# Performance work log

Measured on AMD Instinct MI355X. Metric: run time of the kernel, lower is better.

Reference implementation:

```python
import jax, jax.numpy as jnp
import numpy as np

# cfg.SIAMESE constants (typical FastVOD values)
ROIS_PER_IMAGE = 128
FG_PER_IMAGE = 32          # round(0.25 * 128)
FG_THRESH = 0.7
BG_THRESH_HI = 0.3
BG_THRESH_LO = 0.0

B, N, G = 16, 65536, 64


def _make_boxes(key, shape, img=1000.0):
    k1, k2, k3, k4 = jax.random.split(key, 4)
    x1 = jax.random.uniform(k1, shape) * (img - 64.0)
    y1 = jax.random.uniform(k2, shape) * (img - 64.0)
    w = jax.random.uniform(k3, shape) * 200.0 + 8.0
    h = jax.random.uniform(k4, shape) * 200.0 + 8.0
    return jnp.stack([x1, y1, jnp.minimum(x1 + w, img), jnp.minimum(y1 + h, img)], axis=-1)


def setup_inputs() -> dict:
    key = jax.random.key(0)
    kr, kg, kl, kt, kp, kf, kb, km = jax.random.split(key, 8)
    roi_boxes = _make_boxes(kr, (B, N))                      # [B,N,4]
    all_rois = jnp.concatenate([jnp.zeros((B, N, 1)), roi_boxes], axis=-1)  # [B,N,5]
    gtb = _make_boxes(kg, (B, G))                            # [B,G,4]
    labels = jax.random.randint(kl, (B, G), 1, 31).astype(jnp.float32)
    tids = jax.random.randint(kt, (B, G), 0, 1000).astype(jnp.float32)
    # pad last 8 gt per image with zero boxes (common padding pattern)
    pad = jnp.arange(G) >= G - 8
    gtb = jnp.where(pad[None, :, None], 0.0, gtb)
    labels = jnp.where(pad[None, :], 0.0, labels)
    gt_boxes = jnp.concatenate([gtb, labels[..., None], tids[..., None]], axis=-1)  # [B,G,6]
    u_perm = jax.random.uniform(kp, (B, N + G))
    u_fg = jax.random.uniform(kf, (B, ROIS_PER_IMAGE))
    u_bg = jax.random.uniform(kb, (B, ROIS_PER_IMAGE))
    return {"all_rois": all_rois, "gt_boxes": gt_boxes, "u_perm": u_perm,
            "u_fg": u_fg, "u_bg": u_bg}


def _bbox_overlaps_batch(rois, gt):
    # rois: [B,Nt,5] (idx,x1,y1,x2,y2), gt: [B,G,4]
    a = rois[:, :, 1:5]
    aw = a[:, :, 2] - a[:, :, 0] + 1.0
    ah = a[:, :, 3] - a[:, :, 1] + 1.0
    gw = gt[:, :, 2] - gt[:, :, 0] + 1.0
    gh = gt[:, :, 3] - gt[:, :, 1] + 1.0
    area_a = aw * ah                                  # [B,Nt]
    area_g = gw * gh                                  # [B,G]
    iw = jnp.clip(jnp.minimum(a[:, :, None, 2], gt[:, None, :, 2])
                  - jnp.maximum(a[:, :, None, 0], gt[:, None, :, 0]) + 1.0, 0.0)
    ih = jnp.clip(jnp.minimum(a[:, :, None, 3], gt[:, None, :, 3])
                  - jnp.maximum(a[:, :, None, 1], gt[:, None, :, 1]) + 1.0, 0.0)
    inter = iw * ih                                   # [B,Nt,G]
    ov = inter / (area_a[:, :, None] + area_g[:, None, :] - inter)
    gt_zero = (gw == 1.0) & (gh == 1.0)
    a_zero = (aw == 1.0) & (ah == 1.0)
    ov = jnp.where(gt_zero[:, None, :], 0.0, ov)
    ov = jnp.where(a_zero[:, :, None], -1.0, ov)
    return ov


def _sample_one(max_ov, up, uf, ub):
    # max_ov: [Nt]; replicates the per-image fg/bg sampling loop, vectorized.
    R = ROIS_PER_IMAGE
    fg_mask = max_ov >= FG_THRESH
    bg_mask = ((max_ov < BG_THRESH_HI) & (max_ov >= BG_THRESH_LO)) | (max_ov < 0)
    fg_num = fg_mask.sum()
    bg_num = bg_mask.sum()
    # randomly-ordered fg (resp. bg) indices come first after the argsort
    fg_order = jnp.argsort(jnp.where(fg_mask, up, 2.0))
    bg_order = jnp.argsort(jnp.where(bg_mask, up, 2.0))
    both = (fg_num > 0) & (bg_num > 0)
    only_fg = (fg_num > 0) & (bg_num == 0)
    fg_this = jnp.where(both, jnp.minimum(FG_PER_IMAGE, fg_num),
                        jnp.where(only_fg, R, 0))
    pos = jnp.arange(R)
    # fg: permutation (no replacement) when both present, else uniform w/ replacement
    fg_repl = jnp.clip((uf * fg_num).astype(jnp.int32), 0, jnp.maximum(fg_num - 1, 0))
    fg_pick = jnp.where(only_fg, fg_order[fg_repl], fg_order[pos])
    # bg: always uniform with replacement
    bg_repl = jnp.clip((ub * bg_num).astype(jnp.int32), 0, jnp.maximum(bg_num - 1, 0))
    bg_pick = bg_order[bg_repl]
    is_fg = pos < fg_this
    keep = jnp.where(is_fg, fg_pick, bg_pick)
    return keep, is_fg


def reference(all_rois, gt_boxes, u_perm, u_fg, u_bg):
    # append gt boxes as proposals: [B, N+G, 5]
    gt_append = jnp.concatenate(
        [jnp.zeros_like(gt_boxes[:, :, :1]), gt_boxes[:, :, :4]], axis=-1)
    rois_all = jnp.concatenate([all_rois, gt_append], axis=1)
    ov = _bbox_overlaps_batch(rois_all, gt_boxes[:, :, :4])      # [B,Nt,G]
    max_ov = jnp.max(ov, axis=2)
    gt_assign = jnp.argmax(ov, axis=2)                            # [B,Nt]
    labels = jnp.take_along_axis(gt_boxes[:, :, 4], gt_assign, axis=1)   # [B,Nt]
    tids = jnp.take_along_axis(gt_boxes[:, :, 5], gt_assign, axis=1)
    keep, is_fg = jax.vmap(_sample_one)(max_ov, u_perm, u_fg, u_bg)      # [B,R]
    lab_b = jnp.where(is_fg, jnp.take_along_axis(labels, keep, axis=1), 0.0)
    tid_b = jnp.where(is_fg, jnp.take_along_axis(tids, keep, axis=1), -1.0)
    rois_b = jnp.take_along_axis(rois_all, keep[:, :, None], axis=1)     # [B,R,5]
    batch_idx = jnp.arange(rois_b.shape[0], dtype=rois_b.dtype)[:, None]
    rois_b = rois_b.at[:, :, 0].set(jnp.broadcast_to(batch_idx, rois_b.shape[:2]))
    return rois_b, lab_b, tid_b
```

## Files before the change

### kernel.cpp

```cpp
#include <hip/hip_runtime.h>

#define B_   16
#define N_   65536
#define G_   64
#define M_   (N_ + G_)
#define R_   128
#define FGP  32
#define NB_  16384
#define NCH_ 32
#define CHUNK_ (NB_ / NCH_)
#define NROW_ (B_ * 2)
#define FW_  (NB_ / 32)

__global__ void prep_kernel(const float* __restrict__ gt_boxes,
                            float* __restrict__ gtp)
{
    int t = blockIdx.x * blockDim.x + threadIdx.x;
    if (t >= B_ * G_) return;
    int b = t / G_, j = t % G_;
    const float* g = gt_boxes + t * 6;
    float x1 = g[0], y1 = g[1], x2 = g[2], y2 = g[3];
    float gw = x2 - x1 + 1.0f, gh = y2 - y1 + 1.0f;
    float area = gw * gh;
    bool gz = (gw == 1.0f) && (gh == 1.0f);
    float* o = gtp + b * 5 * G_;
    o[0 * G_ + j] = gz ?  3.0e8f : x1;
    o[1 * G_ + j] = gz ?  3.0e8f : y1;
    o[2 * G_ + j] = gz ? -3.0e8f : x2;
    o[3 * G_ + j] = gz ? -3.0e8f : y2;
    o[4 * G_ + j] = area;
}

__global__ void iou_kernel(const float* __restrict__ all_rois,
                           const float* __restrict__ gt_boxes,
                           const float* __restrict__ gtp,
                           const float* __restrict__ u_perm,
                           unsigned*    __restrict__ packed,
                           int*         __restrict__ hist)
{
    const int b = blockIdx.y;
    const int i = blockIdx.x * blockDim.x + threadIdx.x;
    if (i >= M_) return;

    float x1, y1, x2, y2;
    if (i < N_) {
        const float* p = all_rois + ((size_t)b * N_ + i) * 5;
        x1 = p[1]; y1 = p[2]; x2 = p[3]; y2 = p[4];
    } else {
        const float* p = gt_boxes + (b * G_ + (i - N_)) * 6;
        x1 = p[0]; y1 = p[1]; x2 = p[2]; y2 = p[3];
    }
    float aw = x2 - x1 + 1.0f, ah = y2 - y1 + 1.0f;
    float area_a = aw * ah;
    bool  a_zero = (aw == 1.0f) && (ah == 1.0f);

    const float* gp = gtp + b * 5 * G_;
    float ib = 0.0f, ub = 1.0f;
    #pragma unroll 16
    for (int j = 0; j < G_; ++j) {
        float iw = fminf(x2, gp[2 * G_ + j]) - fmaxf(x1, gp[0 * G_ + j]) + 1.0f;
        float ih = fminf(y2, gp[3 * G_ + j]) - fmaxf(y1, gp[1 * G_ + j]) + 1.0f;
        iw = fmaxf(iw, 0.0f);
        ih = fmaxf(ih, 0.0f);
        float inter = iw * ih;
        float uni   = area_a + gp[4 * G_ + j] - inter;
        float hi1 = inter * ub;
        float lo1 = fmaf(inter, ub, -hi1);
        float hi2 = ib * uni;
        float lo2 = fmaf(ib, uni, -hi2);
        bool gt = (hi1 > hi2) || ((hi1 == hi2) && (lo1 > lo2));
        if (gt) { ib = inter; ub = uni; }
    }
    float best = ib / ub;
    if (a_zero) best = -1.0f;

    bool fg = best >= 0.7f;
    bool bg = best < 0.3f;
    unsigned pk = 0xFFFFFFFFu;
    if (fg || bg) {
        int cls = fg ? 0 : 1;
        float u = u_perm[(size_t)b * M_ + i];
        int bucket = min(max((int)(u * (float)NB_), 0), NB_ - 1);
        pk = ((unsigned)cls << 16) | (unsigned)bucket;
        atomicAdd(&hist[(size_t)(b * 2 + cls) * NB_ + bucket], 1);
    }
    packed[(size_t)b * M_ + i] = pk;
}

__global__ void scan_row(int* __restrict__ hist,
                         int* __restrict__ coarse,
                         int* __restrict__ cnt)
{
    __shared__ int bs[512];
    const int row = blockIdx.x, t = threadIdx.x;
    int4* h4 = (int4*)(hist + (size_t)row * NB_ + t * 32);
    int v[32];
    #pragma unroll
    for (int k = 0; k < 8; ++k) {
        int4 x = h4[k];
        v[k * 4 + 0] = x.x; v[k * 4 + 1] = x.y;
        v[k * 4 + 2] = x.z; v[k * 4 + 3] = x.w;
    }
    int run = 0;
    #pragma unroll
    for (int k = 0; k < 32; ++k) { int x = v[k]; v[k] = run; run += x; }
    bs[t] = run;
    __syncthreads();
    for (int d = 1; d < 512; d <<= 1) {
        int add = (t >= d) ? bs[t - d] : 0;
        __syncthreads();
        bs[t] += add;
        __syncthreads();
    }
    const int texcl = bs[t] - run;
    if ((t & 15) == 15) coarse[row * NCH_ + (t >> 4)] = bs[t];
    if (t == 511) cnt[row] = bs[511];
    #pragma unroll
    for (int k = 0; k < 8; ++k) {
        int4 x;
        x.x = v[k * 4 + 0] + texcl; x.y = v[k * 4 + 1] + texcl;
        x.z = v[k * 4 + 2] + texcl; x.w = v[k * 4 + 3] + texcl;
        h4[k] = x;
    }
}

__global__ void flag_kernel(const float* __restrict__ u_fg,
                            const float* __restrict__ u_bg,
                            const int*  __restrict__ cnt,
                            const int*  __restrict__ coarse,
                            const int*  __restrict__ E,
                            unsigned*   __restrict__ flags,
                            int4*       __restrict__ pick)
{
    __shared__ int sc[2 * NCH_];
    const int b = blockIdx.x;
    const int pos = threadIdx.x;
    if (pos < 2 * NCH_) sc[pos] = coarse[(b * 2) * NCH_ + pos];
    __syncthreads();

    const int fgn = cnt[b * 2 + 0];
    const int bgn = cnt[b * 2 + 1];
    const bool both    = (fgn > 0) && (bgn > 0);
    const bool only_fg = (fgn > 0) && (bgn == 0);
    const int fg_this  = both ? min(FGP, fgn) : (only_fg ? R_ : 0);
    const bool is_fg   = pos < fg_this;

    int cls, rank, cnum;
    if (is_fg) {
        cls = 0; cnum = fgn;
        if (only_fg) {
            float uf = u_fg[b * R_ + pos];
            int kk = (int)(uf * (float)fgn);
            rank = min(max(kk, 0), max(fgn - 1, 0));
        } else {
            rank = pos;
        }
    } else {
        cls = 1; cnum = bgn;
        float ubv = u_bg[b * R_ + pos];
        int kk = (int)(ubv * (float)bgn);
        rank = min(max(kk, 0), max(bgn - 1, 0));
    }

    int4 pk4 = make_int4(0, 0, 0, 0);
    if (cnum > 0) {
        const int row = b * 2 + cls;
        const int* sce = sc + cls * NCH_;
        int c = 0;
        while (c < NCH_ - 1 && sce[c] <= rank) ++c;
        const int* Er = E + (size_t)row * NB_;
        int lo = c * CHUNK_, hi = c * CHUNK_ + CHUNK_ - 1;
        while (lo < hi) {
            int mid = (lo + hi + 1) >> 1;
            if (Er[mid] <= rank) lo = mid; else hi = mid - 1;
        }
        const int start = Er[lo];
        const int next  = (lo < NB_ - 1) ? Er[lo + 1] : cnum;
        atomicOr(&flags[row * FW_ + (lo >> 5)], 1u << (lo & 31));
        pk4 = make_int4(start, next - start, rank - start, lo);
    }
    pick[b * R_ + pos] = pk4;
}

__global__ void scatter_kernel(const unsigned* __restrict__ packed,
                               const unsigned* __restrict__ flags,
                               int*            __restrict__ E,
                               int*            __restrict__ buckets)
{
    const int b = blockIdx.y;
    const int i = blockIdx.x * blockDim.x + threadIdx.x;
    if (i >= M_) return;
    unsigned pk = packed[(size_t)b * M_ + i];
    if (pk == 0xFFFFFFFFu) return;
    const int cls = (int)(pk >> 16);
    const int bucket = (int)(pk & 0xFFFFu);
    const int row = b * 2 + cls;
    unsigned w = flags[row * FW_ + (bucket >> 5)];
    if (!(w & (1u << (bucket & 31)))) return;
    int p = atomicAdd(&E[(size_t)row * NB_ + bucket], 1);
    buckets[(size_t)row * M_ + p] = i;
}

__global__ void sample_kernel(const float* __restrict__ all_rois,
                              const float* __restrict__ gt_boxes,
                              const float* __restrict__ gtp,
                              const float* __restrict__ u_perm,
                              const int*  __restrict__ cnt,
                              const int4* __restrict__ pick,
                              const int*  __restrict__ buckets,
                              float*      __restrict__ out)
{
    const int b   = blockIdx.x;
    const int pos = threadIdx.x;
    const int fgn = cnt[b * 2 + 0];
    const int bgn = cnt[b * 2 + 1];
    const bool both    = (fgn > 0) && (bgn > 0);
    const bool only_fg = (fgn > 0) && (bgn == 0);
    const int fg_this  = both ? min(FGP, fgn) : (only_fg ? R_ : 0);
    const bool is_fg   = pos < fg_this;
    const int cls  = is_fg ? 0 : 1;

    const int4 pk = pick[b * R_ + pos];
    int keep = 0;
    if (pk.y > 0) {
        const int row = b * 2 + cls;
        const int*   be = buckets + (size_t)row * M_ + pk.x;
        const float* up = u_perm + (size_t)b * M_;
        const int cnt2 = pk.y, r = pk.z;
        for (int t2 = 0; t2 < cnt2; ++t2) {
            int it = be[t2]; float ut = up[it];
            int rk = 0;
            for (int s2 = 0; s2 < cnt2; ++s2) {
                if (s2 == t2) continue;
                int is2 = be[s2]; float us = up[is2];
                if (us < ut || (us == ut && is2 < it)) rk++;
            }
            if (rk == r) { keep = it; break; }
        }
    }

    float ox1, oy1, ox2, oy2;
    if (keep < N_) {
        const float* p = all_rois + ((size_t)b * N_ + keep) * 5;
        ox1 = p[1]; oy1 = p[2]; ox2 = p[3]; oy2 = p[4];
    } else {
        const float* p = gt_boxes + (b * G_ + (keep - N_)) * 6;
        ox1 = p[0]; oy1 = p[1]; ox2 = p[2]; oy2 = p[3];
    }
    float* ro = out + ((size_t)b * R_ + pos) * 5;
    ro[0] = (float)b; ro[1] = ox1; ro[2] = oy1; ro[3] = ox2; ro[4] = oy2;

    float lab = 0.0f, tidv = -1.0f;
    if (is_fg) {
        float aw = ox2 - ox1 + 1.0f, ah = oy2 - oy1 + 1.0f;
        float area_a = aw * ah;
        const float* gp = gtp + b * 5 * G_;
        float best = -1e30f;
        int   bi   = 0;
        for (int j = 0; j < G_; ++j) {
            float iw = fminf(ox2, gp[2 * G_ + j]) - fmaxf(ox1, gp[0 * G_ + j]) + 1.0f;
            float ih = fminf(oy2, gp[3 * G_ + j]) - fmaxf(oy1, gp[1 * G_ + j]) + 1.0f;
            iw = fmaxf(iw, 0.0f);
            ih = fmaxf(ih, 0.0f);
            float inter = iw * ih;
            float ov = inter / (area_a + gp[4 * G_ + j] - inter);
            if (ov > best) { best = ov; bi = j; }
        }
        lab  = gt_boxes[(b * G_ + bi) * 6 + 4];
        tidv = gt_boxes[(b * G_ + bi) * 6 + 5];
    }
    float* olab = out + (size_t)B_ * R_ * 5;
    float* otid = olab + (size_t)B_ * R_;
    olab[b * R_ + pos] = lab;
    otid[b * R_ + pos] = tidv;
}

extern "C" void kernel_launch(void* const* d_in, const int* in_sizes, int n_in,
                              void* d_out, int out_size, void* d_ws, size_t ws_size,
                              hipStream_t stream)
{
    const float* all_rois = (const float*)d_in[0];
    const float* gt_boxes = (const float*)d_in[1];
    const float* u_perm   = (const float*)d_in[2];
    const float* u_fg     = (const float*)d_in[3];
    const float* u_bg     = (const float*)d_in[4];
    float* out = (float*)d_out;

    int*      hist    = (int*)d_ws;
    unsigned* flags   = (unsigned*)(hist + (size_t)NROW_ * NB_);
    int*      cnt     = (int*)(flags + NROW_ * FW_);
    int*      coarse  = cnt + 32;
    int4*     pick    = (int4*)(coarse + NROW_ * NCH_);
    unsigned* packed  = (unsigned*)(pick + B_ * R_);
    int*      buckets = (int*)(packed + (size_t)B_ * M_);
    float*    gtp     = (float*)(buckets + (size_t)NROW_ * M_);

    hipMemsetAsync(d_ws, 0, (size_t)(NROW_ * NB_ + NROW_ * FW_) * sizeof(int), stream);

    prep_kernel<<<(B_ * G_ + 255) / 256, 256, 0, stream>>>(gt_boxes, gtp);

    dim3 grid1((M_ + 255) / 256, B_);
    iou_kernel<<<grid1, 256, 0, stream>>>(all_rois, gt_boxes, gtp, u_perm,
                                          packed, hist);
    scan_row<<<NROW_, 512, 0, stream>>>(hist, coarse, cnt);
    flag_kernel<<<B_, R_, 0, stream>>>(u_fg, u_bg, cnt, coarse, hist, flags, pick);
    scatter_kernel<<<grid1, 256, 0, stream>>>(packed, flags, hist, buckets);
    sample_kernel<<<B_, R_, 0, stream>>>(all_rois, gt_boxes, gtp, u_perm,
                                         cnt, pick, buckets, out);
}
```

Before: 95.74 us.

## Stage GT boxes in LDS, skip trailing padded GTs, use wave-shuffle scan

```diff
diff --git a/kernel.cpp b/kernel.cpp
--- a/kernel.cpp
+++ b/kernel.cpp
@@ -13,7 +13,9 @@
 #define FW_  (NB_ / 32)
 
 __global__ void prep_kernel(const float* __restrict__ gt_boxes,
-                            float* __restrict__ gtp)
+                            float4* __restrict__ gt4,
+                            float*  __restrict__ garea,
+                            int*    __restrict__ jmax)
 {
     int t = blockIdx.x * blockDim.x + threadIdx.x;
     if (t >= B_ * G_) return;
@@ -21,25 +23,35 @@
     const float* g = gt_boxes + t * 6;
     float x1 = g[0], y1 = g[1], x2 = g[2], y2 = g[3];
     float gw = x2 - x1 + 1.0f, gh = y2 - y1 + 1.0f;
-    float area = gw * gh;
     bool gz = (gw == 1.0f) && (gh == 1.0f);
-    float* o = gtp + b * 5 * G_;
-    o[0 * G_ + j] = gz ?  3.0e8f : x1;
-    o[1 * G_ + j] = gz ?  3.0e8f : y1;
-    o[2 * G_ + j] = gz ? -3.0e8f : x2;
-    o[3 * G_ + j] = gz ? -3.0e8f : y2;
-    o[4 * G_ + j] = area;
+    gt4[t] = gz ? make_float4(3.0e8f, 3.0e8f, -3.0e8f, -3.0e8f)
+                : make_float4(x1, y1, x2, y2);
+    garea[t] = gw * gh;
+
+    unsigned long long alive = __ballot(!gz);
+    if (j == 0) {
+        int last = 63 - __clzll(alive);
+        jmax[b] = (last + 1 + 7) & ~7;
+    }
 }
 
 __global__ void iou_kernel(const float* __restrict__ all_rois,
                            const float* __restrict__ gt_boxes,
-                           const float* __restrict__ gtp,
-                           const float* __restrict__ u_perm,
-                           unsigned*    __restrict__ packed,
-                           int*         __restrict__ hist)
-{
-    const int b = blockIdx.y;
-    const int i = blockIdx.x * blockDim.x + threadIdx.x;
+                           const float4* __restrict__ gt4,
+                           const float*  __restrict__ garea,
+                           const int*    __restrict__ jmax,
+                           const float*  __restrict__ u_perm,
+                           unsigned*     __restrict__ packed,
+                           int*          __restrict__ hist)
+{
+    __shared__ float4 sg[G_];
+    __shared__ float  sa[G_];
+    const int b   = blockIdx.y;
+    const int tid = threadIdx.x;
+    if (tid < G_) { sg[tid] = gt4[b * G_ + tid]; sa[tid] = garea[b * G_ + tid]; }
+    __syncthreads();
+
+    const int i = blockIdx.x * blockDim.x + tid;
     if (i >= M_) return;
 
     float x1, y1, x2, y2;
@@ -54,22 +66,25 @@
     float area_a = aw * ah;
     bool  a_zero = (aw == 1.0f) && (ah == 1.0f);
 
-    const float* gp = gtp + b * 5 * G_;
+    const int jm = jmax[b];
     float ib = 0.0f, ub = 1.0f;
-    #pragma unroll 16
-    for (int j = 0; j < G_; ++j) {
-        float iw = fminf(x2, gp[2 * G_ + j]) - fmaxf(x1, gp[0 * G_ + j]) + 1.0f;
-        float ih = fminf(y2, gp[3 * G_ + j]) - fmaxf(y1, gp[1 * G_ + j]) + 1.0f;
-        iw = fmaxf(iw, 0.0f);
-        ih = fmaxf(ih, 0.0f);
-        float inter = iw * ih;
-        float uni   = area_a + gp[4 * G_ + j] - inter;
-        float hi1 = inter * ub;
-        float lo1 = fmaf(inter, ub, -hi1);
-        float hi2 = ib * uni;
-        float lo2 = fmaf(ib, uni, -hi2);
-        bool gt = (hi1 > hi2) || ((hi1 == hi2) && (lo1 > lo2));
-        if (gt) { ib = inter; ub = uni; }
+    for (int jj = 0; jj < jm; jj += 8) {
+        #pragma unroll
+        for (int k = 0; k < 8; ++k) {
+            const int j = jj + k;
+            const float4 g  = sg[j];
+            const float  ga = sa[j];
+            float iw = fmaxf(fminf(x2, g.z) - fmaxf(x1, g.x) + 1.0f, 0.0f);
+            float ih = fmaxf(fminf(y2, g.w) - fmaxf(y1, g.y) + 1.0f, 0.0f);
+            float inter = iw * ih;
+            float uni   = area_a + ga - inter;
+            float hi1 = inter * ub;
+            float lo1 = fmaf(inter, ub, -hi1);
+            float hi2 = ib * uni;
+            float lo2 = fmaf(ib, uni, -hi2);
+            bool gt = (hi1 > hi2) || ((hi1 == hi2) && (lo1 > lo2));
+            if (gt) { ib = inter; ub = uni; }
+        }
     }
     float best = ib / ub;
     if (a_zero) best = -1.0f;
@@ -91,36 +106,44 @@
                          int* __restrict__ coarse,
                          int* __restrict__ cnt)
 {
-    __shared__ int bs[512];
+    __shared__ int wt[8], wbase[8];
     const int row = blockIdx.x, t = threadIdx.x;
+    const int lane = t & 63, w = t >> 6;
     int4* h4 = (int4*)(hist + (size_t)row * NB_ + t * 32);
     int v[32];
     #pragma unroll
     for (int k = 0; k < 8; ++k) {
-        int4 x = h4[k];
-        v[k * 4 + 0] = x.x; v[k * 4 + 1] = x.y;
-        v[k * 4 + 2] = x.z; v[k * 4 + 3] = x.w;
+        int4 x4 = h4[k];
+        v[k * 4 + 0] = x4.x; v[k * 4 + 1] = x4.y;
+        v[k * 4 + 2] = x4.z; v[k * 4 + 3] = x4.w;
     }
     int run = 0;
     #pragma unroll
     for (int k = 0; k < 32; ++k) { int x = v[k]; v[k] = run; run += x; }
-    bs[t] = run;
+    int x = run;
+    #pragma unroll
+    for (int d = 1; d < 64; d <<= 1) {
+        int y = __shfl_up(x, d);
+        if (lane >= d) x += y;
+    }
+    if (lane == 63) wt[w] = x;
     __syncthreads();
-    for (int d = 1; d < 512; d <<= 1) {
-        int add = (t >= d) ? bs[t - d] : 0;
-        __syncthreads();
-        bs[t] += add;
-        __syncthreads();
-    }
-    const int texcl = bs[t] - run;
-    if ((t & 15) == 15) coarse[row * NCH_ + (t >> 4)] = bs[t];
-    if (t == 511) cnt[row] = bs[511];
+    if (t == 0) {
+        int acc = 0;
+        #pragma unroll
+        for (int q = 0; q < 8; ++q) { wbase[q] = acc; acc += wt[q]; }
+    }
+    __syncthreads();
+    const int incl  = wbase[w] + x;
+    const int texcl = incl - run;
+    if ((t & 15) == 15) coarse[row * NCH_ + (t >> 4)] = incl;
+    if (t == 511) cnt[row] = incl;
     #pragma unroll
     for (int k = 0; k < 8; ++k) {
-        int4 x;
-        x.x = v[k * 4 + 0] + texcl; x.y = v[k * 4 + 1] + texcl;
-        x.z = v[k * 4 + 2] + texcl; x.w = v[k * 4 + 3] + texcl;
-        h4[k] = x;
+        int4 x4;
+        x4.x = v[k * 4 + 0] + texcl; x4.y = v[k * 4 + 1] + texcl;
+        x4.z = v[k * 4 + 2] + texcl; x4.w = v[k * 4 + 3] + texcl;
+        h4[k] = x4;
     }
 }
 
@@ -203,7 +226,8 @@
 
 __global__ void sample_kernel(const float* __restrict__ all_rois,
                               const float* __restrict__ gt_boxes,
-                              const float* __restrict__ gtp,
+                              const float4* __restrict__ gt4,
+                              const float*  __restrict__ garea,
                               const float* __restrict__ u_perm,
                               const int*  __restrict__ cnt,
                               const int4* __restrict__ pick,
@@ -254,16 +278,15 @@
     if (is_fg) {
         float aw = ox2 - ox1 + 1.0f, ah = oy2 - oy1 + 1.0f;
         float area_a = aw * ah;
-        const float* gp = gtp + b * 5 * G_;
         float best = -1e30f;
         int   bi   = 0;
         for (int j = 0; j < G_; ++j) {
-            float iw = fminf(ox2, gp[2 * G_ + j]) - fmaxf(ox1, gp[0 * G_ + j]) + 1.0f;
-            float ih = fminf(oy2, gp[3 * G_ + j]) - fmaxf(oy1, gp[1 * G_ + j]) + 1.0f;
-            iw = fmaxf(iw, 0.0f);
-            ih = fmaxf(ih, 0.0f);
+            const float4 g  = gt4[b * G_ + j];
+            const float  ga = garea[b * G_ + j];
+            float iw = fmaxf(fminf(ox2, g.z) - fmaxf(ox1, g.x) + 1.0f, 0.0f);
+            float ih = fmaxf(fminf(oy2, g.w) - fmaxf(oy1, g.y) + 1.0f, 0.0f);
             float inter = iw * ih;
-            float ov = inter / (area_a + gp[4 * G_ + j] - inter);
+            float ov = inter / (area_a + ga - inter);
             if (ov > best) { best = ov; bi = j; }
         }
         lab  = gt_boxes[(b * G_ + bi) * 6 + 4];
@@ -293,18 +316,20 @@
     int4*     pick    = (int4*)(coarse + NROW_ * NCH_);
     unsigned* packed  = (unsigned*)(pick + B_ * R_);
     int*      buckets = (int*)(packed + (size_t)B_ * M_);
-    float*    gtp     = (float*)(buckets + (size_t)NROW_ * M_);
+    float4*   gt4     = (float4*)(buckets + (size_t)NROW_ * M_);
+    float*    garea   = (float*)(gt4 + B_ * G_);
+    int*      jmax    = (int*)(garea + B_ * G_);
 
     hipMemsetAsync(d_ws, 0, (size_t)(NROW_ * NB_ + NROW_ * FW_) * sizeof(int), stream);
 
-    prep_kernel<<<(B_ * G_ + 255) / 256, 256, 0, stream>>>(gt_boxes, gtp);
+    prep_kernel<<<(B_ * G_ + 255) / 256, 256, 0, stream>>>(gt_boxes, gt4, garea, jmax);
 
     dim3 grid1((M_ + 255) / 256, B_);
-    iou_kernel<<<grid1, 256, 0, stream>>>(all_rois, gt_boxes, gtp, u_perm,
-                                          packed, hist);
+    iou_kernel<<<grid1, 256, 0, stream>>>(all_rois, gt_boxes, gt4, garea, jmax,
+                                          u_perm, packed, hist);
     scan_row<<<NROW_, 512, 0, stream>>>(hist, coarse, cnt);
     flag_kernel<<<B_, R_, 0, stream>>>(u_fg, u_bg, cnt, coarse, hist, flags, pick);
     scatter_kernel<<<grid1, 256, 0, stream>>>(packed, flags, hist, buckets);
-    sample_kernel<<<B_, R_, 0, stream>>>(all_rois, gt_boxes, gtp, u_perm,
+    sample_kernel<<<B_, R_, 0, stream>>>(all_rois, gt_boxes, gt4, garea, u_perm,
                                          cnt, pick, buckets, out);
 }
```

Result: slower. 99.79 us (+4.2%).
